# Kernel tuning notes

Hardware: AMD Instinct MI355X
Metric: run time of the kernel (lower is better)

Reference implementation:

```python
import jax, jax.numpy as jnp
import numpy as np
from jax import lax

K = 3          # kernel size
PAD = 1        # (K-1)//2
C = 64         # channels
RED = 16       # channel-attention reduction


def conv2d(x, w, b=None):
    # x [B,C,H,W], w [O,I,kh,kw]
    out = lax.conv_general_dilated(x, w, (1, 1), 'SAME',
                                   dimension_numbers=('NCHW', 'OIHW', 'NCHW'))
    if b is not None:
        out = out + b[None, :, None, None]
    return out


def rcab(x, w1, b1, w2, b2, caw1, cab1, caw2, cab2):
    res = conv2d(x, w1, b1)
    res = jax.nn.relu(res)
    res = conv2d(res, w2, b2)
    # channel attention: global avg pool -> 1x1 conv -> relu -> 1x1 conv -> sigmoid
    y = jnp.mean(res, axis=(2, 3), keepdims=True)
    y = jax.nn.relu(conv2d(y, caw1, cab1))
    y = jax.nn.sigmoid(conv2d(y, caw2, cab2))
    return res * y + x


def deform_conv(x, inter, fea, off_w, off_b, mask_w, mask_b, weight):
    # Modulated deformable conv: offsets/mask predicted from concat(inter, fea).
    B, Cc, H, W = x.shape
    KK = K * K
    guide = jnp.concatenate([inter, fea], axis=1)
    offset = conv2d(guide, off_w, off_b)                    # [B, 2*KK, H, W]
    mask = 2.0 * jax.nn.sigmoid(conv2d(guide, mask_w, mask_b))  # [B, KK, H, W]
    off = offset.reshape(B, KK, 2, H, W)
    oy, ox = off[:, :, 0], off[:, :, 1]                     # [B, KK, H, W]

    ky = (jnp.arange(KK) // K - PAD).astype(x.dtype)        # kernel tap y offsets
    kx = (jnp.arange(KK) % K - PAD).astype(x.dtype)
    ii = jnp.arange(H, dtype=x.dtype)[None, None, :, None]
    jj = jnp.arange(W, dtype=x.dtype)[None, None, None, :]
    ys = ii + ky[None, :, None, None] + oy                  # [B, KK, H, W]
    xs = jj + kx[None, :, None, None] + ox

    y0 = jnp.floor(ys); x0 = jnp.floor(xs)
    wy1 = ys - y0; wy0 = 1.0 - wy1
    wx1 = xs - x0; wx0 = 1.0 - wx1
    y0i = y0.astype(jnp.int32); x0i = x0.astype(jnp.int32)
    y1i = y0i + 1; x1i = x0i + 1

    x_flat = x.reshape(B, Cc, H * W)

    def gather(yi, xi):
        valid = ((yi >= 0) & (yi < H) & (xi >= 0) & (xi < W)).astype(x.dtype)
        idx = jnp.clip(yi, 0, H - 1) * W + jnp.clip(xi, 0, W - 1)   # [B,KK,H,W]
        idx = idx.reshape(B, KK * H * W)
        g = jax.vmap(lambda f, i: jnp.take(f, i, axis=1))(x_flat, idx)
        return g.reshape(B, Cc, KK, H, W) * valid[:, None]

    val = (gather(y0i, x0i) * (wy0 * wx0)[:, None]
           + gather(y0i, x1i) * (wy0 * wx1)[:, None]
           + gather(y1i, x0i) * (wy1 * wx0)[:, None]
           + gather(y1i, x1i) * (wy1 * wx1)[:, None])     # [B,C,KK,H,W]
    val = val * mask[:, None]
    w_flat = weight.reshape(weight.shape[0], Cc, KK)        # [O,I,KK]
    return jnp.einsum('bckhw,ock->bohw', val, w_flat)


def setup_inputs() -> dict:
    key = jax.random.key(0)
    ks = jax.random.split(key, 20)
    B, H, W = 4, 192, 192
    f32 = jnp.float32
    d = {
        'x':     jax.random.normal(ks[0], (B, C, H, W), f32),
        'inter': jax.random.normal(ks[1], (B, C, H, W), f32),
        'fea':   jax.random.normal(ks[2], (B, C, H, W), f32),
        # RCAB
        'rcab_w1': jax.random.normal(ks[3], (C, C, 3, 3), f32) * 0.05,
        'rcab_b1': jnp.zeros((C,), f32),
        'rcab_w2': jax.random.normal(ks[4], (C, C, 3, 3), f32) * 0.05,
        'rcab_b2': jnp.zeros((C,), f32),
        'ca_w1': jax.random.normal(ks[5], (C // RED, C, 1, 1), f32) * 0.05,
        'ca_b1': jnp.zeros((C // RED,), f32),
        'ca_w2': jax.random.normal(ks[6], (C, C // RED, 1, 1), f32) * 0.05,
        'ca_b2': jnp.zeros((C,), f32),
        # deformable conv offset/mask branch (input = concat(inter, fea) -> 2C)
        'off_w': jax.random.normal(ks[7], (2 * K * K, 2 * C, 3, 3), f32) * 0.01,
        'off_b': jnp.zeros((2 * K * K,), f32),
        'mask_w': jax.random.normal(ks[8], (K * K, 2 * C, 3, 3), f32) * 0.01,
        'mask_b': jnp.zeros((K * K,), f32),
        'deform_w': jax.random.normal(ks[9], (C, C, K, K), f32) * 0.05,
        # final conv
        'conv_w': jax.random.normal(ks[10], (C, C, 3, 3), f32) * 0.05,
        'conv_b': jnp.zeros((C,), f32),
    }
    return d


def reference(x, inter, fea, rcab_w1, rcab_b1, rcab_w2, rcab_b2,
              ca_w1, ca_b1, ca_w2, ca_b2,
              off_w, off_b, mask_w, mask_b, deform_w, conv_w, conv_b):
    out1 = rcab(x, rcab_w1, rcab_b1, rcab_w2, rcab_b2, ca_w1, ca_b1, ca_w2, ca_b2)
    out2 = deform_conv(out1, inter, fea, off_w, off_b, mask_w, mask_b, deform_w)
    return conv2d(out2 + out1, conv_w, conv_b)
```

## Files before the change

### kernel.cpp

```cpp
#include <hip/hip_runtime.h>
#include <hip/hip_bf16.h>
#include <hip/hip_fp16.h>
#include <math.h>

#define HSZ 192
#define WSZ 192
#define HWSZ (192*192)
#define PH 194
#define PP (PH*PH)
#define NB 4

typedef __attribute__((ext_vector_type(8))) short short8;
typedef __attribute__((ext_vector_type(4))) float f32x4;

__device__ inline unsigned short f2bf(float f) { __hip_bfloat16 h = __float2bfloat16(f); return *(unsigned short*)&h; }
__device__ inline float bf2f(__hip_bfloat16 h) { return __bfloat162float(h); }
__device__ inline float bflo(unsigned u) { return __uint_as_float(u << 16); }
__device__ inline float bfhi(unsigned u) { return __uint_as_float(u & 0xffff0000u); }

#define GLDS(SRC, DST) __builtin_amdgcn_global_load_lds( \
    (const __attribute__((address_space(1))) unsigned int*)(const void*)(SRC), \
    (__attribute__((address_space(3))) unsigned int*)(void*)(DST), 16, 0, 0)

#define MFMA(A,B,C) __builtin_amdgcn_mfma_f32_16x16x32_bf16((A),(B),(C),0,0,0)

__global__ void zb2_k(__hip_bfloat16* xn, __hip_bfloat16* r1, __hip_bfloat16* res,
                      __hip_bfloat16* cat) {
  int job = blockIdx.y;
  __hip_bfloat16* buf = job == 0 ? xn : job == 1 ? r1 : job == 2 ? res : cat;
  int Cn = (job == 3) ? 128 : 64;
  int cg8 = Cn >> 3;
  int tot = NB * 772 * cg8;
  int idx = blockIdx.x * 256 + threadIdx.x;
  if (idx >= tot) return;
  int cg = idx % cg8; int rem = idx / cg8;
  int e = rem % 772; int b = rem / 772;
  int h, w2;
  if (e < 194) { h = 0; w2 = e; }
  else if (e < 388) { h = 193; w2 = e - 194; }
  else if (e < 580) { h = e - 388 + 1; w2 = 0; }
  else { h = e - 580 + 1; w2 = 193; }
  uint4 z = make_uint4(0, 0, 0, 0);
  *(uint4*)&buf[(((size_t)b * PH + h) * PH + w2) * Cn + cg * 8] = z;
}

__global__ void wts_k(const float* __restrict__ rw1, const float* __restrict__ rw2,
                      const float* __restrict__ cw, const float* __restrict__ offw,
                      const float* __restrict__ maskw, const float* __restrict__ offb,
                      const float* __restrict__ maskb, const float* __restrict__ dwv,
                      short* wt1, short* wt2c, short* wtf, short* wtom, float* ob,
                      short* wtb, float* meanz) {
  int job = blockIdx.y;
  int idx = blockIdx.x * 256 + threadIdx.x;
  if (job < 3) {
    const float* src = job == 0 ? rw1 : job == 1 ? rw2 : cw;
    short* dst = job == 0 ? wt1 : job == 1 ? wt2c : wtf;
    int kk = idx >> 12, rem = idx & 4095;
    int co = rem >> 6, ci = rem & 63;
    dst[idx] = (short)f2bf(src[(co * 64 + ci) * 9 + kk]);
  } else if (job == 3) {
    int kk = idx >> 12, rem = idx & 4095;
    int co = rem >> 7, ci = rem & 127;
    float v = 0.f;
    if (co < 18) v = offw[(co * 128 + ci) * 9 + kk];
    else if (co < 27) v = maskw[((co - 18) * 128 + ci) * 9 + kk];
    wtom[idx] = (short)f2bf(v);
    if (idx < 32) ob[idx] = idx < 18 ? offb[idx] : (idx < 27 ? maskb[idx - 18] : 0.f);
  } else {
    int o = idx / 576, rem = idx - o * 576;
    int kk = rem >> 6, ci = rem & 63;
    wtb[idx] = (short)f2bf(dwv[(o * 64 + ci) * 9 + kk]);
    if (blockIdx.x == 0 && threadIdx.x < 256) meanz[threadIdx.x] = 0.f;
  }
}

__global__ __launch_bounds__(256) void cvt_k(const float* __restrict__ x,
    const float* __restrict__ inter, const float* __restrict__ fea,
    __hip_bfloat16* __restrict__ xn, __hip_bfloat16* __restrict__ cat) {
  int job = blockIdx.z;
  const float* src = job == 0 ? x : job == 1 ? inter : fea;
  __hip_bfloat16* dst = job == 0 ? xn : cat;
  int Cdst = job == 0 ? 64 : 128;
  int coff = job == 2 ? 64 : 0;
  __shared__ float s[64][65];
  int p0 = blockIdx.x * 64; int b = blockIdx.y;
  int lane = threadIdx.x & 63, g = threadIdx.x >> 6;
#pragma unroll
  for (int i = 0; i < 16; ++i) {
    int c = i * 4 + g;
    s[c][lane] = src[((size_t)b * 64 + c) * HWSZ + p0 + lane];
  }
  __syncthreads();
  int pix = threadIdx.x >> 2, cg = threadIdx.x & 3;
  int h = p0 / WSZ, w0 = p0 - h * WSZ + pix;
  size_t addr = (((size_t)b * PH + h + 1) * PH + 1 + w0) * Cdst + coff + cg * 16;
  unsigned pk2[8];
#pragma unroll
  for (int t = 0; t < 8; ++t)
    pk2[t] = (unsigned)f2bf(s[cg * 16 + 2 * t][pix]) | ((unsigned)f2bf(s[cg * 16 + 2 * t + 1][pix]) << 16);
  *(uint4*)&dst[addr]     = make_uint4(pk2[0], pk2[1], pk2[2], pk2[3]);
  *(uint4*)&dst[addr + 8] = make_uint4(pk2[4], pk2[5], pk2[6], pk2[7]);
}

template<int OUT_MODE, bool RELU, bool MEANACC>
__global__ __launch_bounds__(512, 3) void conv_mfma_k(
    const __hip_bfloat16* __restrict__ inp, const short* __restrict__ wt,
    const float* __restrict__ bias, __hip_bfloat16* __restrict__ outB,
    float* __restrict__ outF, float* __restrict__ meanout) {
  __shared__ __align__(16) short tbuf[2 * 12800];
  __shared__ float smean[256];
  int flat = ((int)blockIdx.x & 7) * 96 + ((int)blockIdx.x >> 3);
  const int b = flat / 192, h = flat - (flat / 192) * 192;
  const int tid = threadIdx.x, lane = tid & 63, wid = tid >> 6;
  const int q = lane >> 4, r16 = lane & 15;
  const int cw = wid >> 2;
  const int wm0 = (wid & 3) * 48;

  const __hip_bfloat16* base = inp + ((size_t)b * PH + h) * (PH * 64);
#define STAGE(BUF, R) do { \
    const char* gb_ = (const char*)(base + (size_t)(R) * (PH * 64)); \
    for (int s_ = wid; s_ < 25; s_ += 8) { \
      int pix_ = 8 * s_ + (lane >> 3); \
      const char* src_ = gb_ + pix_ * 128 + ((((lane & 7) ^ ((lane >> 3) & 7))) << 4); \
      GLDS(src_, tbuf + (BUF) * 12800 + s_ * 512); \
    } \
  } while (0)

  STAGE(0, 0);

  f32x4 acc[3][2];
  if (OUT_MODE == 0) {
#pragma unroll
    for (int nf = 0; nf < 2; ++nf) {
      float4 bv = *(const float4*)&bias[(cw * 2 + nf) * 16 + q * 4];
      f32x4 v; v[0] = bv.x; v[1] = bv.y; v[2] = bv.z; v[3] = bv.w;
      acc[0][nf] = v; acc[1][nf] = v; acc[2][nf] = v;
    }
  } else {
#pragma unroll
    for (int nf = 0; nf < 2; ++nf) {
      float bs = bias[(cw * 2 + nf) * 16 + r16];
      f32x4 v; v[0] = bs; v[1] = bs; v[2] = bs; v[3] = bs;
      acc[0][nf] = v; acc[1][nf] = v; acc[2][nf] = v;
    }
  }

  short8 bfr[2][2][2];
  {
    const short* wk0 = wt + r16 * 64 + q * 8;
#pragma unroll
    for (int nf = 0; nf < 2; ++nf) {
      bfr[0][0][nf] = *(const short8*)(wk0 + (cw * 2 + nf) * 1024);
      bfr[0][1][nf] = *(const short8*)(wk0 + (cw * 2 + nf) * 1024 + 32);
    }
  }
  __syncthreads();

#pragma unroll
  for (int ky = 0; ky < 3; ++ky) {
    const int cb = ky & 1;
    if (ky < 2) STAGE(cb ^ 1, ky + 1);
#pragma unroll
    for (int kx = 0; kx < 3; ++kx) {
      const int kk = ky * 3 + kx;
      const int cur = kk & 1;
      if (kk < 8) {
        const short* wk = wt + (kk + 1) * 4096 + r16 * 64 + q * 8;
#pragma unroll
        for (int nf = 0; nf < 2; ++nf) {
          bfr[cur ^ 1][0][nf] = *(const short8*)(wk + (cw * 2 + nf) * 1024);
          bfr[cur ^ 1][1][nf] = *(const short8*)(wk + (cw * 2 + nf) * 1024 + 32);
        }
      }
#pragma unroll
      for (int mf = 0; mf < 3; ++mf) {
        int pix = wm0 + mf * 16 + r16 + kx;
        const char* ab = (const char*)(tbuf + cb * 12800) + pix * 128;
        int sw = (pix & 7) << 4;
        short8 a0 = *(const short8*)(ab + ((q << 4) ^ sw));
        short8 a1 = *(const short8*)(ab + (((q + 4) << 4) ^ sw));
#pragma unroll
        for (int nf = 0; nf < 2; ++nf) {
          if (OUT_MODE == 0) {
            acc[mf][nf] = MFMA(bfr[cur][0][nf], a0, acc[mf][nf]);
            acc[mf][nf] = MFMA(bfr[cur][1][nf], a1, acc[mf][nf]);
          } else {
            acc[mf][nf] = MFMA(a0, bfr[cur][0][nf], acc[mf][nf]);
            acc[mf][nf] = MFMA(a1, bfr[cur][1][nf], acc[mf][nf]);
          }
        }
      }
    }
    __syncthreads();
  }
#undef STAGE

  if (MEANACC) {
    float t[2][4];
#pragma unroll
    for (int nf = 0; nf < 2; ++nf)
#pragma unroll
      for (int rg = 0; rg < 4; ++rg)
        t[nf][rg] = acc[0][nf][rg] + acc[1][nf][rg] + acc[2][nf][rg];
#pragma unroll
    for (int m = 1; m < 16; m <<= 1)
#pragma unroll
      for (int nf = 0; nf < 2; ++nf)
#pragma unroll
        for (int rg = 0; rg < 4; ++rg)
          t[nf][rg] += __shfl_xor(t[nf][rg], m);
    if (r16 == 0)
#pragma unroll
      for (int nf = 0; nf < 2; ++nf)
#pragma unroll
        for (int rg = 0; rg < 4; ++rg)
          smean[wid * 32 + nf * 16 + q * 4 + rg] = t[nf][rg];
    __syncthreads();
    if (tid < 64) {
      int half = tid >> 5, cl = tid & 31;
      atomicAdd(&meanout[b * 64 + tid],
                (smean[(half * 4 + 0) * 32 + cl] + smean[(half * 4 + 1) * 32 + cl] +
                 smean[(half * 4 + 2) * 32 + cl] + smean[(half * 4 + 3) * 32 + cl]) * (1.f / 36864.f));
    }
  }

  if (OUT_MODE == 0) {
    short* t1 = tbuf + 12800;
#pragma unroll
    for (int mf = 0; mf < 3; ++mf)
#pragma unroll
      for (int nf = 0; nf < 2; ++nf) {
        f32x4 v = acc[mf][nf];
        if (RELU) { v[0] = fmaxf(v[0], 0.f); v[1] = fmaxf(v[1], 0.f); v[2] = fmaxf(v[2], 0.f); v[3] = fmaxf(v[3], 0.f); }
        unsigned lo = (unsigned)f2bf(v[0]) | ((unsigned)f2bf(v[1]) << 16);
        unsigned hi = (unsigned)f2bf(v[2]) | ((unsigned)f2bf(v[3]) << 16);
        int pix = wm0 + mf * 16 + r16;
        int byteoff = (pix * 128 + (cw * 2 + nf) * 32 + q * 8) ^ ((pix & 7) << 4);
        *(uint2*)((char*)t1 + byteoff) = make_uint2(lo, hi);
      }
    __syncthreads();
    char* orow = (char*)outB + ((((size_t)b * PH + h + 1) * PH + 1) * 64) * 2;
    for (int s = wid; s < 24; s += 8) {
      int pix = 8 * s + (lane >> 3);
      int g16 = ((lane & 7) ^ (pix & 7)) << 4;
      uint4 d = *(const uint4*)((const char*)t1 + pix * 128 + g16);
      *(uint4*)(orow + pix * 128 + ((lane & 7) << 4)) = d;
    }
  } else {
    float* ob2 = outF + (size_t)b * 64 * HWSZ + h * WSZ;
#pragma unroll
    for (int mf = 0; mf < 3; ++mf)
#pragma unroll
      for (int nf = 0; nf < 2; ++nf) {
        int pix0 = wm0 + mf * 16 + q * 4;
        int co = (cw * 2 + nf) * 16 + r16;
        *(f32x4*)&ob2[(size_t)co * HWSZ + pix0] = acc[mf][nf];
      }
  }
}

__global__ __launch_bounds__(512, 3) void offmask_mfma_k(
    const __hip_bfloat16* __restrict__ cat, const short* __restrict__ wt2,
    const float* __restrict__ ob, float* __restrict__ om) {
  int flat = ((int)blockIdx.x & 7) * 96 + ((int)blockIdx.x >> 3);
  const int b = flat / 192, h = flat - (flat / 192) * 192;
  const int tid = threadIdx.x, lane = tid & 63, wid = tid >> 6;
  const int q = lane >> 4, r16 = lane & 15;
  const int cw = wid >> 2;
  const int wm0 = (wid & 3) * 48;
  __shared__ __align__(16) short tile[200 * 128];

  f32x4 acc[3];
  {
    float bs = ob[cw * 16 + r16];
    f32x4 v; v[0] = bs; v[1] = bs; v[2] = bs; v[3] = bs;
    acc[0] = v; acc[1] = v; acc[2] = v;
  }
  const char* gb = (const char*)(cat + ((size_t)b * PH + h) * (PH * 128));

  short8 bfr[2][4];
  {
    const short* wk0 = wt2 + cw * 2048 + r16 * 128 + q * 8;
#pragma unroll
    for (int c4 = 0; c4 < 4; ++c4)
      bfr[0][c4] = *(const short8*)(wk0 + c4 * 32);
  }

#pragma unroll
  for (int r = 0; r < 3; ++r) {
    __syncthreads();
    for (int s = wid; s < 50; s += 8) {
      int pix = 4 * s + (lane >> 4);
      const char* src = gb + (size_t)r * (PH * 256) + pix * 256
                      + ((((lane & 15) ^ (pix & 15))) << 4);
      GLDS(src, tile + s * 512);
    }
    __syncthreads();
#pragma unroll
    for (int kx = 0; kx < 3; ++kx) {
      const int kk = r * 3 + kx;
      const int cur = kk & 1;
      if (kk < 8) {
        const short* wk = wt2 + (kk + 1) * 4096 + cw * 2048 + r16 * 128 + q * 8;
#pragma unroll
        for (int c4 = 0; c4 < 4; ++c4)
          bfr[cur ^ 1][c4] = *(const short8*)(wk + c4 * 32);
      }
#pragma unroll
      for (int mf = 0; mf < 3; ++mf) {
        int pix = wm0 + mf * 16 + r16 + kx;
        const char* ab = (const char*)tile + pix * 256;
        int sw = (pix & 15) << 4;
        short8 a0 = *(const short8*)(ab + ((q << 4) ^ sw));
        short8 a1 = *(const short8*)(ab + (((4 + q) << 4) ^ sw));
        short8 a2 = *(const short8*)(ab + (((8 + q) << 4) ^ sw));
        short8 a3 = *(const short8*)(ab + (((12 + q) << 4) ^ sw));
        acc[mf] = MFMA(a0, bfr[cur][0], acc[mf]);
        acc[mf] = MFMA(a1, bfr[cur][1], acc[mf]);
        acc[mf] = MFMA(a2, bfr[cur][2], acc[mf]);
        acc[mf] = MFMA(a3, bfr[cur][3], acc[mf]);
      }
    }
  }
  int co = cw * 16 + r16;
  if (co < 27) {
#pragma unroll
    for (int mf = 0; mf < 3; ++mf) {
      f32x4 v = acc[mf];
      if (co >= 18) {
        v[0] = 2.f / (1.f + expf(-v[0])); v[1] = 2.f / (1.f + expf(-v[1]));
        v[2] = 2.f / (1.f + expf(-v[2])); v[3] = 2.f / (1.f + expf(-v[3]));
      }
      *(f32x4*)&om[((size_t)(b * 27 + co)) * HWSZ + h * WSZ + wm0 + mf * 16 + q * 4] = v;
    }
  }
}

__global__ __launch_bounds__(256) void out1_k(__hip_bfloat16* __restrict__ res, const __hip_bfloat16* __restrict__ xn,
    const float* __restrict__ mean, const float* __restrict__ w1, const float* __restrict__ b1,
    const float* __restrict__ w2, const float* __restrict__ b2) {
  int idx = blockIdx.x * 256 + threadIdx.x;
  int b = idx / 294912; int rem = idx - b * 294912;
  int p = rem >> 3, c8 = rem & 7;
  int lane = threadIdx.x & 63, wid = threadIdx.x >> 6;

  __shared__ float s_t[4];
  {
    float prod = w1[wid * 64 + lane] * mean[b * 64 + lane];
#pragma unroll
    for (int m = 1; m < 64; m <<= 1) prod += __shfl_xor(prod, m);
    if (lane == 0) s_t[wid] = fmaxf(prod + b1[wid], 0.f);
  }
  __syncthreads();
  float t0 = s_t[0], t1 = s_t[1], t2 = s_t[2], t3 = s_t[3];

  int hh = p / WSZ, ww = p - hh * WSZ;
  size_t off = ((size_t)b * PP + (size_t)(hh + 1) * PH + ww + 1) * 64 + c8 * 8;
  __hip_bfloat16* rp = res + off;
  const __hip_bfloat16* xp = xn + off;
  unsigned pk[4];
#pragma unroll
  for (int t = 0; t < 4; ++t) {
    float y0, y1;
    {
      int c = c8 * 8 + 2 * t;
      const float4 wv0 = *(const float4*)&w2[c * 4];
      const float4 wv1 = *(const float4*)&w2[(c + 1) * 4];
      float v0 = b2[c]     + wv0.x * t0 + wv0.y * t1 + wv0.z * t2 + wv0.w * t3;
      float v1 = b2[c + 1] + wv1.x * t0 + wv1.y * t1 + wv1.z * t2 + wv1.w * t3;
      y0 = 1.f / (1.f + expf(-v0));
      y1 = 1.f / (1.f + expf(-v1));
    }
    float o0 = bf2f(rp[2 * t]) * y0 + bf2f(xp[2 * t]);
    float o1 = bf2f(rp[2 * t + 1]) * y1 + bf2f(xp[2 * t + 1]);
    pk[t] = (unsigned)f2bf(o0) | ((unsigned)f2bf(o1) << 16);
  }
  *(uint4*)rp = make_uint4(pk[0], pk[1], pk[2], pk[3]);
}

__global__ __launch_bounds__(256) void deform_mfma_k(
    const __hip_bfloat16* __restrict__ nhwc, const float* __restrict__ om,
    const short* __restrict__ wtb, __hip_bfloat16* __restrict__ fin) {
  int blk = ((int)blockIdx.x & 7) * 288 + ((int)blockIdx.x >> 3);
  int b = blk / 576;
  int p0 = (blk - b * 576) * 64;
  int tid = threadIdx.x, lane = tid & 63, wid = tid >> 6;
  int q = lane >> 4, r16 = lane & 15;
  __shared__ __align__(16) short sA[2][64][64];
  __shared__ __half2 s_bw[2][9][64];
  __shared__ int s_pk[9][64];

  const float* omb = om + (size_t)b * 27 * HWSZ + p0;
  for (int e = tid; e < 576; e += 256) {
    int kk = e >> 6, pix = e & 63;
    int p = p0 + pix;
    int h = p / WSZ, w2 = p - h * WSZ;
    float oy = omb[(size_t)(2 * kk) * HWSZ + pix];
    float ox = omb[(size_t)(2 * kk + 1) * HWSZ + pix];
    float m2 = omb[(size_t)(18 + kk) * HWSZ + pix];
    float ys = (float)(h + kk / 3 - 1) + oy;
    float xs = (float)(w2 + kk % 3 - 1) + ox;
    float y0f = floorf(ys), x0f = floorf(xs);
    float wy1 = ys - y0f, wx1 = xs - x0f;
    float wy0 = 1.f - wy1, wx0 = 1.f - wx1;
    int y0 = (int)y0f, x0i = (int)x0f;
    int y1 = y0 + 1, x1 = x0i + 1;
    float vy0 = (y0 >= 0 && y0 < HSZ) ? 1.f : 0.f;
    float vx0 = (x0i >= 0 && x0i < WSZ) ? 1.f : 0.f;
    float vy1 = (y1 >= 0 && y1 < HSZ) ? 1.f : 0.f;
    float vx1 = (x1 >= 0 && x1 < WSZ) ? 1.f : 0.f;
    int y0c = min(max(y0, 0), HSZ - 1), x0c = min(max(x0i, 0), WSZ - 1);
    int y1c = min(max(y1, 0), HSZ - 1), x1c = min(max(x1, 0), WSZ - 1);
    s_bw[0][kk][pix] = __floats2half2_rn(wy0 * wx0 * m2 * vy0 * vx0, wy0 * wx1 * m2 * vy0 * vx1);
    s_bw[1][kk][pix] = __floats2half2_rn(wy1 * wx0 * m2 * vy1 * vx0, wy1 * wx1 * m2 * vy1 * vx1);
    s_pk[kk][pix] = ((((y0c + 1) * PH) + x0c + 1) << 2) | ((y1c - y0c) << 1) | (x1c - x0c);
  }
  __syncthreads();

  const __hip_bfloat16* nb = nhwc + (size_t)b * PP * 64;
  const int spix = tid >> 2, lg = tid & 3;
  const int rsw = (r16 & 7) << 4;

  uint4 Pa0, Pb0, Qa0, Qb0, Ra0, Rb0, Sa0, Sb0;
  uint4 Pa1, Pb1, Qa1, Qb1, Ra1, Rb1, Sa1, Sb1;
  float2 wab0, wcd0, wab1, wcd1;

#define ISSUE_R(KK, Pa,Pb,Qa,Qb,Ra,Rb,Sa,Sb, Wab, Wcd) do { \
    Wab = __half22float2(s_bw[0][KK][spix]); \
    Wcd = __half22float2(s_bw[1][KK][spix]); \
    int pk_ = s_pk[KK][spix]; \
    int i00_ = pk_ >> 2, dy_ = (pk_ >> 1) & 1, dx_ = pk_ & 1; \
    const __hip_bfloat16* g_ = nb + (size_t)i00_ * 64 + lg * 16; \
    Pa = *(const uint4*)g_;                     Pb = *(const uint4*)(g_ + 8); \
    Qa = *(const uint4*)(g_ + dx_ * 64);        Qb = *(const uint4*)(g_ + dx_ * 64 + 8); \
    Ra = *(const uint4*)(g_ + dy_ * (PH * 64)); Rb = *(const uint4*)(g_ + dy_ * (PH * 64) + 8); \
    Sa = *(const uint4*)(g_ + (dy_ * PH + dx_) * 64); Sb = *(const uint4*)(g_ + (dy_ * PH + dx_) * 64 + 8); \
  } while (0)
#define CMB(J, PA,QA,RA,SA, Wab, Wcd, OUT) do { \
    const unsigned* pa_ = (const unsigned*)&PA; const unsigned* qa_ = (const unsigned*)&QA; \
    const unsigned* ra_ = (const unsigned*)&RA; const unsigned* sa_ = (const unsigned*)&SA; \
    float lo_ = Wab.x * bflo(pa_[J]) + Wab.y * bflo(qa_[J]) + Wcd.x * bflo(ra_[J]) + Wcd.y * bflo(sa_[J]); \
    float hi_ = Wab.x * bfhi(pa_[J]) + Wab.y * bfhi(qa_[J]) + Wcd.x * bfhi(ra_[J]) + Wcd.y * bfhi(sa_[J]); \
    OUT = (unsigned)f2bf(lo_) | ((unsigned)f2bf(hi_) << 16); \
  } while (0)
#define CSTORE_R(BUFOFF, Pa,Pb,Qa,Qb,Ra,Rb,Sa,Sb, Wab, Wcd) do { \
    unsigned oa_[4], ob_[4]; \
    CMB(0, Pa,Qa,Ra,Sa, Wab, Wcd, oa_[0]); CMB(1, Pa,Qa,Ra,Sa, Wab, Wcd, oa_[1]); \
    CMB(2, Pa,Qa,Ra,Sa, Wab, Wcd, oa_[2]); CMB(3, Pa,Qa,Ra,Sa, Wab, Wcd, oa_[3]); \
    CMB(0, Pb,Qb,Rb,Sb, Wab, Wcd, ob_[0]); CMB(1, Pb,Qb,Rb,Sb, Wab, Wcd, ob_[1]); \
    CMB(2, Pb,Qb,Rb,Sb, Wab, Wcd, ob_[2]); CMB(3, Pb,Qb,Rb,Sb, Wab, Wcd, ob_[3]); \
    char* dst_ = (char*)sA + (BUFOFF) + spix * 128; \
    *(uint4*)(dst_ + ((((lg * 2) ^ (spix & 7))) << 4))     = make_uint4(oa_[0], oa_[1], oa_[2], oa_[3]); \
    *(uint4*)(dst_ + ((((lg * 2 + 1) ^ (spix & 7))) << 4)) = make_uint4(ob_[0], ob_[1], ob_[2], ob_[3]); \
  } while (0)

  ISSUE_R(0, Pa0,Pb0,Qa0,Qb0,Ra0,Rb0,Sa0,Sb0, wab0, wcd0);
  CSTORE_R(0, Pa0,Pb0,Qa0,Qb0,Ra0,Rb0,Sa0,Sb0, wab0, wcd0);
  ISSUE_R(1, Pa0,Pb0,Qa0,Qb0,Ra0,Rb0,Sa0,Sb0, wab0, wcd0);
  ISSUE_R(2, Pa1,Pb1,Qa1,Qb1,Ra1,Rb1,Sa1,Sb1, wab1, wcd1);

  f32x4 acc0 = (f32x4){0.f, 0.f, 0.f, 0.f};
  f32x4 acc1 = (f32x4){0.f, 0.f, 0.f, 0.f};
  f32x4 acc2 = (f32x4){0.f, 0.f, 0.f, 0.f};
  f32x4 acc3 = (f32x4){0.f, 0.f, 0.f, 0.f};
  const short* wrow = wtb + (size_t)(wid * 16 + r16) * 576;
  const char* a0base = (const char*)sA + r16 * 128;
  const char* a1base = (const char*)sA + (r16 + 16) * 128;
  const char* a2base = (const char*)sA + (r16 + 32) * 128;
  const char* a3base = (const char*)sA + (r16 + 48) * 128;

#pragma unroll
  for (int kk = 0; kk < 9; ++kk) {
    const int bo = (kk & 1) * 8192;
    __syncthreads();
#pragma unroll
    for (int s = 0; s < 2; ++s) {
      short8 wf = *(const short8*)(wrow + kk * 64 + s * 32 + q * 8);
      int off = bo + ((s * 64 + q * 16) ^ rsw);
      acc0 = MFMA(wf, *(const short8*)(a0base + off), acc0);
      acc1 = MFMA(wf, *(const short8*)(a1base + off), acc1);
      acc2 = MFMA(wf, *(const short8*)(a2base + off), acc2);
      acc3 = MFMA(wf, *(const short8*)(a3base + off), acc3);
    }
    if (kk < 8) {
      const int nbo = ((kk + 1) & 1) * 8192;
      if ((kk & 1) == 0) {
        CSTORE_R(nbo, Pa0,Pb0,Qa0,Qb0,Ra0,Rb0,Sa0,Sb0, wab0, wcd0);
        if (kk + 3 <= 8) ISSUE_R(kk + 3, Pa0,Pb0,Qa0,Qb0,Ra0,Rb0,Sa0,Sb0, wab0, wcd0);
      } else {
        CSTORE_R(nbo, Pa1,Pb1,Qa1,Qb1,Ra1,Rb1,Sa1,Sb1, wab1, wcd1);
        if (kk + 3 <= 8) ISSUE_R(kk + 3, Pa1,Pb1,Qa1,Qb1,Ra1,Rb1,Sa1,Sb1, wab1, wcd1);
      }
    }
  }

  int h0 = p0 / WSZ, w0 = p0 - h0 * WSZ;
  size_t ro = ((size_t)(h0 + 1) * PH + w0 + 1) * 64;
  const __hip_bfloat16* resid = nb + ro;
  __hip_bfloat16* fp = fin + (size_t)b * PP * 64 + ro;
#pragma unroll
  for (int nf = 0; nf < 4; ++nf) {
    f32x4 av = nf == 0 ? acc0 : nf == 1 ? acc1 : nf == 2 ? acc2 : acc3;
    int pix = r16 + nf * 16;
    int co = wid * 16 + q * 4;
    const unsigned* rr = (const unsigned*)(resid + (size_t)pix * 64 + co);
    unsigned r0 = rr[0], r1 = rr[1];
    float o0 = av[0] + bflo(r0);
    float o1 = av[1] + bfhi(r0);
    float o2 = av[2] + bflo(r1);
    float o3 = av[3] + bfhi(r1);
    uint2 pk2 = make_uint2((unsigned)f2bf(o0) | ((unsigned)f2bf(o1) << 16),
                           (unsigned)f2bf(o2) | ((unsigned)f2bf(o3) << 16));
    *(uint2*)(fp + (size_t)pix * 64 + co) = pk2;
  }
#undef ISSUE_R
#undef CMB
#undef CSTORE_R
}

extern "C" void kernel_launch(void* const* d_in, const int* in_sizes, int n_in,
                              void* d_out, int out_size, void* d_ws, size_t ws_size,
                              hipStream_t stream) {
  (void)in_sizes; (void)n_in; (void)out_size; (void)ws_size;
  const float* x     = (const float*)d_in[0];
  const float* inter = (const float*)d_in[1];
  const float* fea   = (const float*)d_in[2];
  const float* rw1   = (const float*)d_in[3];
  const float* rb1   = (const float*)d_in[4];
  const float* rw2   = (const float*)d_in[5];
  const float* rb2   = (const float*)d_in[6];
  const float* caw1  = (const float*)d_in[7];
  const float* cab1  = (const float*)d_in[8];
  const float* caw2  = (const float*)d_in[9];
  const float* cab2  = (const float*)d_in[10];
  const float* offw  = (const float*)d_in[11];
  const float* offb  = (const float*)d_in[12];
  const float* maskw = (const float*)d_in[13];
  const float* maskb = (const float*)d_in[14];
  const float* dw    = (const float*)d_in[15];
  const float* cw    = (const float*)d_in[16];
  const float* cb    = (const float*)d_in[17];

  char* w = (char*)d_ws;
  const size_t P64 = (size_t)NB * PP * 64 * 2 + 4096;
  const size_t PCAT = (size_t)NB * PP * 128 * 2 + 4096;
  __hip_bfloat16* xn   = (__hip_bfloat16*)(w);
  __hip_bfloat16* r1   = (__hip_bfloat16*)(w + P64);
  __hip_bfloat16* res  = (__hip_bfloat16*)(w + 2 * P64);
  float* omb           = (float*)(w + 3 * P64);
  __hip_bfloat16* cat  = (__hip_bfloat16*)(w + 4 * P64);
  char* tail = w + 4 * P64 + PCAT;
  short* wt1  = (short*)tail; tail += 73728;
  short* wt2c = (short*)tail; tail += 73728;
  short* wtf  = (short*)tail; tail += 73728;
  short* wtom = (short*)tail; tail += 73728;
  float* obb  = (float*)tail; tail += 128;
  short* wtb  = (short*)tail; tail += 73728;
  float* mean = (float*)tail; tail += 1024;
  __hip_bfloat16* fin = r1;

  zb2_k<<<dim3(194, 4), 256, 0, stream>>>(xn, r1, res, cat);
  wts_k<<<dim3(144, 5), 256, 0, stream>>>(rw1, rw2, cw, offw, maskw, offb, maskb, dw,
                                          wt1, wt2c, wtf, wtom, obb, wtb, mean);
  cvt_k<<<dim3(576, 4, 3), 256, 0, stream>>>(x, inter, fea, xn, cat);

  conv_mfma_k<0, true , false><<<768, 512, 0, stream>>>(xn, wt1, rb1, r1, nullptr, nullptr);
  conv_mfma_k<0, false, true ><<<768, 512, 0, stream>>>(r1, wt2c, rb2, res, nullptr, mean);
  out1_k<<<4608, 256, 0, stream>>>(res, xn, mean, caw1, cab1, caw2, cab2);
  offmask_mfma_k<<<768, 512, 0, stream>>>(cat, wtom, obb, omb);
  deform_mfma_k<<<NB * 576, 256, 0, stream>>>(res, omb, wtb, fin);
  conv_mfma_k<1, false, false><<<768, 512, 0, stream>>>(fin, wtf, cb, nullptr, (float*)d_out, nullptr);
}
```

Before: 247.5 us.

## Make deform MFMA waves own their pixels to remove block barriers

Reassigns work in the deformable-conv MFMA kernel so each wave owns 16 pixels end to end: the offset/mask precompute, the bilinear gather into shared memory and the MFMA all use that wave's own pixel rows, with each wave now covering all 64 output channels. This removes the __syncthreads after the precompute and the one inside every kernel-tap iteration. The cost is that each wave loads weight fragments for all four channel groups from global memory instead of one. Correctness relies on the wave running in lockstep for its own shared-memory writes and reads.

```diff
diff --git a/kernel.cpp b/kernel.cpp
--- a/kernel.cpp
+++ b/kernel.cpp
@@ -391,8 +391,9 @@
   __shared__ int s_pk[9][64];
 
   const float* omb = om + (size_t)b * 27 * HWSZ + p0;
-  for (int e = tid; e < 576; e += 256) {
-    int kk = e >> 6, pix = e & 63;
+  for (int t = lane; t < 144; t += 64) {
+    int kk = t >> 4, pixl = t & 15;
+    int pix = wid * 16 + pixl;
     int p = p0 + pix;
     int h = p / WSZ, w2 = p - h * WSZ;
     float oy = omb[(size_t)(2 * kk) * HWSZ + pix];
@@ -415,10 +416,9 @@
     s_bw[1][kk][pix] = __floats2half2_rn(wy1 * wx0 * m2 * vy1 * vx0, wy1 * wx1 * m2 * vy1 * vx1);
     s_pk[kk][pix] = ((((y0c + 1) * PH) + x0c + 1) << 2) | ((y1c - y0c) << 1) | (x1c - x0c);
   }
-  __syncthreads();
 
   const __hip_bfloat16* nb = nhwc + (size_t)b * PP * 64;
-  const int spix = tid >> 2, lg = tid & 3;
+  const int spix = wid * 16 + (lane >> 2), lg = lane & 3;
   const int rsw = (r16 & 7) << 4;
 
   uint4 Pa0, Pb0, Qa0, Qb0, Ra0, Rb0, Sa0, Sb0;
@@ -463,25 +463,27 @@
   f32x4 acc1 = (f32x4){0.f, 0.f, 0.f, 0.f};
   f32x4 acc2 = (f32x4){0.f, 0.f, 0.f, 0.f};
   f32x4 acc3 = (f32x4){0.f, 0.f, 0.f, 0.f};
-  const short* wrow = wtb + (size_t)(wid * 16 + r16) * 576;
-  const char* a0base = (const char*)sA + r16 * 128;
-  const char* a1base = (const char*)sA + (r16 + 16) * 128;
-  const char* a2base = (const char*)sA + (r16 + 32) * 128;
-  const char* a3base = (const char*)sA + (r16 + 48) * 128;
+  const char* abase = (const char*)sA + (wid * 16 + r16) * 128;
+  const short* wr0 = wtb + (size_t)(0 * 16 + r16) * 576 + q * 8;
+  const short* wr1 = wtb + (size_t)(1 * 16 + r16) * 576 + q * 8;
+  const short* wr2 = wtb + (size_t)(2 * 16 + r16) * 576 + q * 8;
+  const short* wr3 = wtb + (size_t)(3 * 16 + r16) * 576 + q * 8;
 
 #pragma unroll
   for (int kk = 0; kk < 9; ++kk) {
     const int bo = (kk & 1) * 8192;
-    __syncthreads();
-#pragma unroll
-    for (int s = 0; s < 2; ++s) {
-      short8 wf = *(const short8*)(wrow + kk * 64 + s * 32 + q * 8);
-      int off = bo + ((s * 64 + q * 16) ^ rsw);
-      acc0 = MFMA(wf, *(const short8*)(a0base + off), acc0);
-      acc1 = MFMA(wf, *(const short8*)(a1base + off), acc1);
-      acc2 = MFMA(wf, *(const short8*)(a2base + off), acc2);
-      acc3 = MFMA(wf, *(const short8*)(a3base + off), acc3);
-    }
+    const int off0 = bo + ((q * 16) ^ rsw);
+    const int off1 = bo + ((64 + q * 16) ^ rsw);
+    short8 va0 = *(const short8*)(abase + off0);
+    short8 va1 = *(const short8*)(abase + off1);
+    acc0 = MFMA(*(const short8*)(wr0 + kk * 64), va0, acc0);
+    acc0 = MFMA(*(const short8*)(wr0 + kk * 64 + 32), va1, acc0);
+    acc1 = MFMA(*(const short8*)(wr1 + kk * 64), va0, acc1);
+    acc1 = MFMA(*(const short8*)(wr1 + kk * 64 + 32), va1, acc1);
+    acc2 = MFMA(*(const short8*)(wr2 + kk * 64), va0, acc2);
+    acc2 = MFMA(*(const short8*)(wr2 + kk * 64 + 32), va1, acc2);
+    acc3 = MFMA(*(const short8*)(wr3 + kk * 64), va0, acc3);
+    acc3 = MFMA(*(const short8*)(wr3 + kk * 64 + 32), va1, acc3);
     if (kk < 8) {
       const int nbo = ((kk + 1) & 1) * 8192;
       if ((kk & 1) == 0) {
@@ -496,14 +498,14 @@
 
   int h0 = p0 / WSZ, w0 = p0 - h0 * WSZ;
   size_t ro = ((size_t)(h0 + 1) * PH + w0 + 1) * 64;
-  const __hip_bfloat16* resid = nb + ro;
-  __hip_bfloat16* fp = fin + (size_t)b * PP * 64 + ro;
-#pragma unroll
-  for (int nf = 0; nf < 4; ++nf) {
-    f32x4 av = nf == 0 ? acc0 : nf == 1 ? acc1 : nf == 2 ? acc2 : acc3;
-    int pix = r16 + nf * 16;
-    int co = wid * 16 + q * 4;
-    const unsigned* rr = (const unsigned*)(resid + (size_t)pix * 64 + co);
+  int pix = wid * 16 + r16;
+  const __hip_bfloat16* resid = nb + ro + (size_t)pix * 64;
+  __hip_bfloat16* fp = fin + (size_t)b * PP * 64 + ro + (size_t)pix * 64;
+#pragma unroll
+  for (int cf = 0; cf < 4; ++cf) {
+    f32x4 av = cf == 0 ? acc0 : cf == 1 ? acc1 : cf == 2 ? acc2 : acc3;
+    int co = cf * 16 + q * 4;
+    const unsigned* rr = (const unsigned*)(resid + co);
     unsigned r0 = rr[0], r1 = rr[1];
     float o0 = av[0] + bflo(r0);
     float o1 = av[1] + bfhi(r0);
@@ -511,7 +513,7 @@
     float o3 = av[3] + bfhi(r1);
     uint2 pk2 = make_uint2((unsigned)f2bf(o0) | ((unsigned)f2bf(o1) << 16),
                            (unsigned)f2bf(o2) | ((unsigned)f2bf(o3) << 16));
-    *(uint2*)(fp + (size_t)pix * 64 + co) = pk2;
+    *(uint2*)(fp + co) = pk2;
   }
 #undef ISSUE_R
 #undef CMB
```

Result: slower. 307.2 us (+24.2%).
